# Performance work log

Measured on AMD Instinct MI355X. Metric: run time of the kernel, lower is better.

Reference implementation:

```python
import jax, jax.numpy as jnp
import numpy as np

B, N, M, D, H = 2, 4096, 4096, 512, 8
P = D // H


def setup_inputs() -> dict:
    key = jax.random.key(0)
    ks = jax.random.split(key, 9)
    s = 1.0 / np.sqrt(D)
    return {
        "queries": jax.random.normal(ks[0], (B, N, D), dtype=jnp.float32),
        "keys": jax.random.normal(ks[1], (B, M, D), dtype=jnp.float32),
        "values": jax.random.normal(ks[2], (B, M, D), dtype=jnp.float32),
        "Wq": jax.random.normal(ks[3], (D, D), dtype=jnp.float32) * s,
        "bq": jax.random.normal(ks[4], (D,), dtype=jnp.float32) * s,
        "Wk": jax.random.normal(ks[5], (D, D), dtype=jnp.float32) * s,
        "bk": jax.random.normal(ks[6], (D,), dtype=jnp.float32) * s,
        "Wv": jax.random.normal(ks[7], (D, D), dtype=jnp.float32) * s,
        "bv": jax.random.normal(ks[8], (D,), dtype=jnp.float32) * s,
    }


def reference(queries, keys, values, Wq, bq, Wk, bk, Wv, bv):
    b, n, d = queries.shape
    m = keys.shape[1]
    h, p = H, D // H
    temperature = jnp.asarray(p, queries.dtype) ** 0.5
    # Linear projections (torch Linear: x @ W^T + b; here W stored as [in, out])
    q = (queries @ Wq + bq).reshape(b, n, h, p)
    k = (keys @ Wk + bk).reshape(b, m, h, p)
    v = (values @ Wv + bv).reshape(b, m, h, p)
    # scaled dot-product attention per head; scores [b, h, n, m]
    scores = jnp.einsum("bnhp,bmhp->bhnm", q, k) / temperature
    attn = jax.nn.softmax(scores, axis=-1)
    out = jnp.einsum("bhnm,bmhp->bnhp", attn, v)
    return out.reshape(b, n, d)
```

## Files before the change

kernel.cpp:

```cpp
#include <hip/hip_runtime.h>
#include <stdint.h>

#define B_ 2
#define N_ 4096
#define M_ 4096
#define D_ 512
#define H_ 8
#define P_ 64

typedef short bf16x8 __attribute__((ext_vector_type(8)));
typedef float f32x4 __attribute__((ext_vector_type(4)));
typedef unsigned short u16;
typedef unsigned int u32;
typedef u32 u32x4 __attribute__((ext_vector_type(4)));

static __device__ __forceinline__ u16 f2bf(float f) {
  u32 u = __builtin_bit_cast(u32, f);
  u32 r = u + 0x7fffu + ((u >> 16) & 1u);
  return (u16)(r >> 16);
}

static __device__ __forceinline__ u32 cvtpk(float lo, float hi_) {
  u32 d;
  asm("v_cvt_pk_bf16_f32 %0, %1, %2" : "=v"(d) : "v"(lo), "v"(hi_));
  return d;
}

static __device__ __forceinline__ float fexp2(float x) {
  float r;
  asm("v_exp_f32 %0, %1" : "=v"(r) : "v"(x));
  return r;
}

static __device__ __forceinline__ u32 permpk(const bf16x8& a0, const bf16x8& a1, int i) {
  u32x4 a0w = __builtin_bit_cast(u32x4, a0);
  u32x4 a1w = __builtin_bit_cast(u32x4, a1);
  int wd = i >> 1;
  u32 sel = (i & 1) ? 0x07060302u : 0x05040100u;
  return __builtin_amdgcn_perm(a1w[wd], a0w[wd], sel);
}

__global__ __launch_bounds__(256) void wt_kernel(const float* __restrict__ Wq,
                                                 const float* __restrict__ Wk,
                                                 const float* __restrict__ Wv,
                                                 u16* __restrict__ Wt) {
  __shared__ float tile[32][33];
  int z = blockIdx.z;
  const float* W = (z == 0) ? Wq : (z == 1) ? Wk : Wv;
  u16* out = Wt + (size_t)z * D_ * D_;
  int o0 = blockIdx.x * 32, d0 = blockIdx.y * 32;
  int tx = threadIdx.x, ty = threadIdx.y;
#pragma unroll
  for (int k = 0; k < 4; k++) tile[ty + k * 8][tx] = W[(size_t)(d0 + ty + k * 8) * D_ + o0 + tx];
  __syncthreads();
#pragma unroll
  for (int k = 0; k < 4; k++) out[(size_t)(o0 + ty + k * 8) * D_ + d0 + tx] = f2bf(tile[tx][ty + k * 8]);
}

__global__ __launch_bounds__(256) void proj_kernel(const float* __restrict__ Xq,
                                                   const float* __restrict__ Xk,
                                                   const float* __restrict__ Xv,
                                                   const u16* __restrict__ Wt,
                                                   const float* __restrict__ bq,
                                                   const float* __restrict__ bk,
                                                   const float* __restrict__ bv,
                                                   u16* __restrict__ QKV) {
  int z = blockIdx.z;
  const float* X = (z == 0) ? Xq : (z == 1) ? Xk : Xv;
  const float* bias = (z == 0) ? bq : (z == 1) ? bk : bv;
  const u16* W = Wt + (size_t)z * D_ * D_;
  u16* Y = QKV + (size_t)z * (B_ * N_ * D_);
  const float scale = (z == 0) ? 0.18033688011112042f : 1.0f;

  __shared__ u16 Alds[128 * 32];
  __shared__ u16 Blds[128 * 32];

  int t = threadIdx.x;
  int lane = t & 63, w = t >> 6;
  int wm = w >> 1, wn = w & 1;
  int l15 = lane & 15, g = lane >> 4;
  int rb = blockIdx.y * 128, ob = blockIdx.x * 128;

  const f32x4 zero4 = {0.f, 0.f, 0.f, 0.f};
  f32x4 acc[4][4];
#pragma unroll
  for (int m = 0; m < 4; m++)
#pragma unroll
    for (int n = 0; n < 4; n++) acc[m][n] = zero4;

  for (int kb = 0; kb < D_; kb += 32) {
    __syncthreads();
#pragma unroll
    for (int i = 0; i < 4; i++) {
      int chunk = t + i * 256;
      int row = chunk >> 3, c4 = chunk & 7;
      const float4 v = *(const float4*)&X[(size_t)(rb + row) * D_ + kb + c4 * 4];
      u32 lo = (u32)f2bf(v.x) | ((u32)f2bf(v.y) << 16);
      u32 hi = (u32)f2bf(v.z) | ((u32)f2bf(v.w) << 16);
      int byte = row * 64 + ((c4 * 8) ^ ((row & 3) << 4));
      uint2 d;
      d.x = lo;
      d.y = hi;
      *(uint2*)((char*)Alds + byte) = d;
    }
#pragma unroll
    for (int i = 0; i < 2; i++) {
      int chunk = t + i * 256;
      int row = chunk >> 2, c = chunk & 3;
      bf16x8 v = *(const bf16x8*)&W[(size_t)(ob + row) * D_ + kb + c * 8];
      int byte = row * 64 + ((c * 16) ^ ((row & 3) << 4));
      *(bf16x8*)((char*)Blds + byte) = v;
    }
    __syncthreads();

    bf16x8 a[4], b[4];
#pragma unroll
    for (int m = 0; m < 4; m++) {
      int row = wm * 64 + m * 16 + l15;
      int byte = row * 64 + ((g * 16) ^ ((row & 3) << 4));
      a[m] = *(const bf16x8*)((char*)Alds + byte);
    }
#pragma unroll
    for (int n = 0; n < 4; n++) {
      int row = wn * 64 + n * 16 + l15;
      int byte = row * 64 + ((g * 16) ^ ((row & 3) << 4));
      b[n] = *(const bf16x8*)((char*)Blds + byte);
    }
#pragma unroll
    for (int m = 0; m < 4; m++)
#pragma unroll
      for (int n = 0; n < 4; n++)
        acc[m][n] = __builtin_amdgcn_mfma_f32_16x16x32_bf16(a[m], b[n], acc[m][n], 0, 0, 0);
  }

#pragma unroll
  for (int n = 0; n < 4; n++) {
    int col = ob + wn * 64 + n * 16 + l15;
    float bv_ = bias[col];
#pragma unroll
    for (int m = 0; m < 4; m++) {
      int row0 = rb + wm * 64 + m * 16 + g * 4;
#pragma unroll
      for (int r = 0; r < 4; r++) {
        float y = (acc[m][n][r] + bv_) * scale;
        Y[(size_t)(row0 + r) * D_ + col] = f2bf(y);
      }
    }
  }
}

__global__ __launch_bounds__(256, 2) void attn_kernel(const u16* __restrict__ QKV,
                                                      float* __restrict__ out) {
  const u16* Q = QKV;
  const u16* K = QKV + (size_t)(B_ * N_ * D_);
  const u16* V = K + (size_t)(B_ * N_ * D_);

  __shared__ u16 Klds[2][64 * 64];
  __shared__ u16 Vlds[2][64 * 64];

  char* KL = (char*)&Klds[0][0];
  char* VL = (char*)&Vlds[0][0];

  int t = threadIdx.x, l = t & 63, w = t >> 6;
  int l15 = l & 15, g = (l >> 4) & 3;
  int swz = (l15 & 7) << 4;

  int bid = blockIdx.x + 32 * (blockIdx.y + 8 * blockIdx.z);
  int sbid = (bid & 7) * 64 + (bid >> 3);
  int qt = sbid & 31, h = (sbid >> 5) & 7, b = sbid >> 8;
  int qwa = qt * 128 + w * 16;
  int qwb = qwa + 64;

  const u16* Kb = K + (size_t)(b * M_) * D_ + h * P_;
  const u16* Vb = V + (size_t)(b * M_) * D_ + h * P_;

  bf16x8 qfa[2], qfb[2];
  const u16* qrow_a = Q + (size_t)(b * N_ + qwa + l15) * D_ + h * P_;
  const u16* qrow_b = Q + (size_t)(b * N_ + qwb + l15) * D_ + h * P_;
#pragma unroll
  for (int step = 0; step < 2; step++) {
    qfa[step] = *(const bf16x8*)(qrow_a + step * 32 + g * 8);
    qfb[step] = *(const bf16x8*)(qrow_b + step * 32 + g * 8);
  }

  int koff0 = l15 * 128 + ((g * 16) ^ swz);
  int koff1 = l15 * 128 + ((64 + g * 16) ^ swz);
  int voff0 = koff0, voff1 = koff1;
  int krow = t >> 3, kc = t & 7;
  int kwoff = krow * 128 + ((kc * 16) ^ ((krow & 7) << 4));
  const u16* kg0 = Kb + (size_t)krow * D_ + kc * 8;
  const u16* kg1 = kg0 + (size_t)32 * D_;
  int kp = t & 31, p0 = (t >> 5) * 8;
  int kv0 = 2 * kp, blk = kv0 >> 5, ww_ = kv0 & 31;
  int slot = blk * 32 + ((ww_ >> 2) & 3) * 8 + ((ww_ >> 4) << 2) + (ww_ & 3);
  int vwB = p0 * 128 + 2 * slot;
  const u16* vg0 = Vb + (size_t)kv0 * D_ + p0;
  const u16* vg1 = vg0 + D_;

  const f32x4 zero4 = {0.f, 0.f, 0.f, 0.f};
  const u32x4 onesw = {0x3F803F80u, 0x3F803F80u, 0x3F803F80u, 0x3F803F80u};
  const bf16x8 ones_f = __builtin_bit_cast(bf16x8, onesw);
  f32x4 oa[4], ob_[4], ol_a = zero4, ol_b = zero4;
#pragma unroll
  for (int i = 0; i < 4; i++) {
    oa[i] = zero4;
    ob_[i] = zero4;
  }

  {
    *(bf16x8*)(KL + kwoff) = *(const bf16x8*)kg0;
    *(bf16x8*)(KL + kwoff + 4096) = *(const bf16x8*)kg1;
    bf16x8 a0 = *(const bf16x8*)vg0;
    bf16x8 a1 = *(const bf16x8*)vg1;
#pragma unroll
    for (int i = 0; i < 8; i++) *(u32*)(VL + ((vwB ^ (i << 4)) + i * 128)) = permpk(a0, a1, i);
  }
  kwoff ^= 0x2000;
  vwB ^= 0x2000;
  const u16* kgp0 = kg0 + (size_t)64 * D_;
  const u16* kgp1 = kg1 + (size_t)64 * D_;
  const u16* vgp0 = vg0 + (size_t)64 * D_;
  const u16* vgp1 = vg1 + (size_t)64 * D_;
  __syncthreads();

  const int NT = M_ / 64;
  for (int kt = 0; kt < NT; kt++) {
    bf16x8 kn0 = {}, kn1 = {}, vn0 = {}, vn1 = {};
    if (kt + 1 < NT) {
      kn0 = *(const bf16x8*)kgp0;
      kn1 = *(const bf16x8*)kgp1;
      vn0 = *(const bf16x8*)vgp0;
      vn1 = *(const bf16x8*)vgp1;
      kgp0 += (size_t)64 * D_;
      kgp1 += (size_t)64 * D_;
      vgp0 += (size_t)64 * D_;
      vgp1 += (size_t)64 * D_;
    }

    f32x4 sa[4], sb[4];
#pragma unroll
    for (int i = 0; i < 4; i++) {
      sa[i] = zero4;
      sb[i] = zero4;
    }
    __builtin_amdgcn_s_setprio(1);
#pragma unroll
    for (int tt = 0; tt < 4; tt++) {
      bf16x8 kf0 = *(const bf16x8*)(KL + koff0 + tt * 2048);
      sa[tt] = __builtin_amdgcn_mfma_f32_16x16x32_bf16(kf0, qfa[0], sa[tt], 0, 0, 0);
      sb[tt] = __builtin_amdgcn_mfma_f32_16x16x32_bf16(kf0, qfb[0], sb[tt], 0, 0, 0);
      bf16x8 kf1 = *(const bf16x8*)(KL + koff1 + tt * 2048);
      sa[tt] = __builtin_amdgcn_mfma_f32_16x16x32_bf16(kf1, qfa[1], sa[tt], 0, 0, 0);
      sb[tt] = __builtin_amdgcn_mfma_f32_16x16x32_bf16(kf1, qfb[1], sb[tt], 0, 0, 0);
    }
    __builtin_amdgcn_s_setprio(0);

#pragma unroll
    for (int tt = 0; tt < 4; tt++)
#pragma unroll
      for (int r = 0; r < 4; r++) {
        sa[tt][r] = fexp2(sa[tt][r]);
        sb[tt][r] = fexp2(sb[tt][r]);
      }

    u32 pwa[2][4], pwb[2][4];
#pragma unroll
    for (int kb2 = 0; kb2 < 2; kb2++)
#pragma unroll
      for (int wd = 0; wd < 4; wd++) {
        const f32x4& sva = sa[2 * kb2 + (wd >> 1)];
        const f32x4& svb = sb[2 * kb2 + (wd >> 1)];
        pwa[kb2][wd] = cvtpk(sva[(wd & 1) * 2], sva[(wd & 1) * 2 + 1]);
        pwb[kb2][wd] = cvtpk(svb[(wd & 1) * 2], svb[(wd & 1) * 2 + 1]);
      }

    __builtin_amdgcn_s_setprio(1);
#pragma unroll
    for (int kb2 = 0; kb2 < 2; kb2++) {
      u32x4 pva = {pwa[kb2][0], pwa[kb2][1], pwa[kb2][2], pwa[kb2][3]};
      u32x4 pvb = {pwb[kb2][0], pwb[kb2][1], pwb[kb2][2], pwb[kb2][3]};
      bf16x8 pfa = __builtin_bit_cast(bf16x8, pva);
      bf16x8 pfb = __builtin_bit_cast(bf16x8, pvb);
      int voff = kb2 ? voff1 : voff0;
#pragma unroll
      for (int tt = 0; tt < 4; tt++) {
        bf16x8 vf = *(const bf16x8*)(VL + voff + tt * 2048);
        oa[tt] = __builtin_amdgcn_mfma_f32_16x16x32_bf16(vf, pfa, oa[tt], 0, 0, 0);
        ob_[tt] = __builtin_amdgcn_mfma_f32_16x16x32_bf16(vf, pfb, ob_[tt], 0, 0, 0);
      }
      ol_a = __builtin_amdgcn_mfma_f32_16x16x32_bf16(ones_f, pfa, ol_a, 0, 0, 0);
      ol_b = __builtin_amdgcn_mfma_f32_16x16x32_bf16(ones_f, pfb, ol_b, 0, 0, 0);
    }
    __builtin_amdgcn_s_setprio(0);

    if (kt + 1 < NT) {
      *(bf16x8*)(KL + kwoff) = kn0;
      *(bf16x8*)(KL + kwoff + 4096) = kn1;
#pragma unroll
      for (int i = 0; i < 8; i++) *(u32*)(VL + ((vwB ^ (i << 4)) + i * 128)) = permpk(vn0, vn1, i);
    }
    koff0 ^= 0x2000;
    koff1 ^= 0x2000;
    voff0 ^= 0x2000;
    voff1 ^= 0x2000;
    kwoff ^= 0x2000;
    vwB ^= 0x2000;
    __syncthreads();
  }

  float rla = 1.0f / ol_a[0], rlb = 1.0f / ol_b[0];
  float* orow_a = out + (size_t)(b * N_ + qwa + l15) * D_ + h * P_;
  float* orow_b = out + (size_t)(b * N_ + qwb + l15) * D_ + h * P_;
#pragma unroll
  for (int tt = 0; tt < 4; tt++) {
    float4 sta = {oa[tt][0] * rla, oa[tt][1] * rla, oa[tt][2] * rla, oa[tt][3] * rla};
    *(float4*)(orow_a + tt * 16 + g * 4) = sta;
    float4 stb = {ob_[tt][0] * rlb, ob_[tt][1] * rlb, ob_[tt][2] * rlb, ob_[tt][3] * rlb};
    *(float4*)(orow_b + tt * 16 + g * 4) = stb;
  }
}

extern "C" void kernel_launch(void* const* d_in, const int* in_sizes, int n_in,
                              void* d_out, int out_size, void* d_ws, size_t ws_size,
                              hipStream_t stream) {
  const float* queries = (const float*)d_in[0];
  const float* keys = (const float*)d_in[1];
  const float* values = (const float*)d_in[2];
  const float* Wq = (const float*)d_in[3];
  const float* bq = (const float*)d_in[4];
  const float* Wk = (const float*)d_in[5];
  const float* bk = (const float*)d_in[6];
  const float* Wv = (const float*)d_in[7];
  const float* bv = (const float*)d_in[8];
  float* out = (float*)d_out;

  u16* QKV = (u16*)d_ws;
  u16* Wt = QKV + (size_t)3 * B_ * N_ * D_;

  wt_kernel<<<dim3(16, 16, 3), dim3(32, 8), 0, stream>>>(Wq, Wk, Wv, Wt);
  proj_kernel<<<dim3(4, 64, 3), 256, 0, stream>>>(queries, keys, values, Wt, bq, bk, bv, QKV);
  attn_kernel<<<dim3(32, 8, 2), 256, 0, stream>>>(QKV, out);
}
```

Measured before the change: 119.1 us.

## Double attention block to 512 threads and split K/V tile loading across halves

The attention kernel now runs 8 waves per block covering 256 query rows, half the previous number of blocks, so each K/V tile staged in LDS serves twice as many queries. The first 256 threads load K and the second 256 load and permute V, which halves the per-thread global loads and LDS stores. The score MFMAs now take the zero accumulator directly instead of zeroing registers first. In exchange the grid shrinks to 256 blocks, which can leave some of the GPU's compute units idle, and the launch bound of 512 threads with 2 blocks per CU constrains registers.

```diff
diff --git a/kernel.cpp b/kernel.cpp
--- a/kernel.cpp
+++ b/kernel.cpp
@@ -149,7 +149,7 @@
   }
 }
 
-__global__ __launch_bounds__(256, 2) void attn_kernel(const u16* __restrict__ QKV,
+__global__ __launch_bounds__(512, 2) void attn_kernel(const u16* __restrict__ QKV,
                                                       float* __restrict__ out) {
   const u16* Q = QKV;
   const u16* K = QKV + (size_t)(B_ * N_ * D_);
@@ -165,11 +165,11 @@
   int l15 = l & 15, g = (l >> 4) & 3;
   int swz = (l15 & 7) << 4;
 
-  int bid = blockIdx.x + 32 * (blockIdx.y + 8 * blockIdx.z);
-  int sbid = (bid & 7) * 64 + (bid >> 3);
-  int qt = sbid & 31, h = (sbid >> 5) & 7, b = sbid >> 8;
-  int qwa = qt * 128 + w * 16;
-  int qwb = qwa + 64;
+  int bid = blockIdx.x + 16 * (blockIdx.y + 8 * blockIdx.z);
+  int sbid = (bid & 7) * 32 + (bid >> 3);
+  int qt = sbid & 15, h = (sbid >> 4) & 7, b = sbid >> 7;
+  int qwa = qt * 256 + w * 16;
+  int qwb = qwa + 128;
 
   const u16* Kb = K + (size_t)(b * M_) * D_ + h * P_;
   const u16* Vb = V + (size_t)(b * M_) * D_ + h * P_;
@@ -186,30 +186,34 @@
   int koff0 = l15 * 128 + ((g * 16) ^ swz);
   int koff1 = l15 * 128 + ((64 + g * 16) ^ swz);
   int voff0 = koff0, voff1 = koff1;
-  int krow = t >> 3, kc = t & 7;
+
+  int th = t & 255;
+  bool isK = (t < 256);
+  int krow = th >> 3, kc = th & 7;
   int kwoff = krow * 128 + ((kc * 16) ^ ((krow & 7) << 4));
   const u16* kg0 = Kb + (size_t)krow * D_ + kc * 8;
   const u16* kg1 = kg0 + (size_t)32 * D_;
-  int kp = t & 31, p0 = (t >> 5) * 8;
+  int kp = th & 31, p0 = (th >> 5) * 8;
   int kv0 = 2 * kp, blk = kv0 >> 5, ww_ = kv0 & 31;
   int slot = blk * 32 + ((ww_ >> 2) & 3) * 8 + ((ww_ >> 4) << 2) + (ww_ & 3);
   int vwB = p0 * 128 + 2 * slot;
   const u16* vg0 = Vb + (size_t)kv0 * D_ + p0;
   const u16* vg1 = vg0 + D_;
 
-  const f32x4 zero4 = {0.f, 0.f, 0.f, 0.f};
+  const f32x4 zc = {0.f, 0.f, 0.f, 0.f};
   const u32x4 onesw = {0x3F803F80u, 0x3F803F80u, 0x3F803F80u, 0x3F803F80u};
   const bf16x8 ones_f = __builtin_bit_cast(bf16x8, onesw);
-  f32x4 oa[4], ob_[4], ol_a = zero4, ol_b = zero4;
+  f32x4 oa[4], ob_[4], ol_a = zc, ol_b = zc;
 #pragma unroll
   for (int i = 0; i < 4; i++) {
-    oa[i] = zero4;
-    ob_[i] = zero4;
-  }
-
-  {
+    oa[i] = zc;
+    ob_[i] = zc;
+  }
+
+  if (isK) {
     *(bf16x8*)(KL + kwoff) = *(const bf16x8*)kg0;
     *(bf16x8*)(KL + kwoff + 4096) = *(const bf16x8*)kg1;
+  } else {
     bf16x8 a0 = *(const bf16x8*)vg0;
     bf16x8 a1 = *(const bf16x8*)vg1;
 #pragma unroll
@@ -225,12 +229,15 @@
 
   const int NT = M_ / 64;
   for (int kt = 0; kt < NT; kt++) {
-    bf16x8 kn0 = {}, kn1 = {}, vn0 = {}, vn1 = {};
+    bf16x8 n0 = {}, n1 = {};
     if (kt + 1 < NT) {
-      kn0 = *(const bf16x8*)kgp0;
-      kn1 = *(const bf16x8*)kgp1;
-      vn0 = *(const bf16x8*)vgp0;
-      vn1 = *(const bf16x8*)vgp1;
+      if (isK) {
+        n0 = *(const bf16x8*)kgp0;
+        n1 = *(const bf16x8*)kgp1;
+      } else {
+        n0 = *(const bf16x8*)vgp0;
+        n1 = *(const bf16x8*)vgp1;
+      }
       kgp0 += (size_t)64 * D_;
       kgp1 += (size_t)64 * D_;
       vgp0 += (size_t)64 * D_;
@@ -238,17 +245,12 @@
     }
 
     f32x4 sa[4], sb[4];
-#pragma unroll
-    for (int i = 0; i < 4; i++) {
-      sa[i] = zero4;
-      sb[i] = zero4;
-    }
     __builtin_amdgcn_s_setprio(1);
 #pragma unroll
     for (int tt = 0; tt < 4; tt++) {
       bf16x8 kf0 = *(const bf16x8*)(KL + koff0 + tt * 2048);
-      sa[tt] = __builtin_amdgcn_mfma_f32_16x16x32_bf16(kf0, qfa[0], sa[tt], 0, 0, 0);
-      sb[tt] = __builtin_amdgcn_mfma_f32_16x16x32_bf16(kf0, qfb[0], sb[tt], 0, 0, 0);
+      sa[tt] = __builtin_amdgcn_mfma_f32_16x16x32_bf16(kf0, qfa[0], zc, 0, 0, 0);
+      sb[tt] = __builtin_amdgcn_mfma_f32_16x16x32_bf16(kf0, qfb[0], zc, 0, 0, 0);
       bf16x8 kf1 = *(const bf16x8*)(KL + koff1 + tt * 2048);
       sa[tt] = __builtin_amdgcn_mfma_f32_16x16x32_bf16(kf1, qfa[1], sa[tt], 0, 0, 0);
       sb[tt] = __builtin_amdgcn_mfma_f32_16x16x32_bf16(kf1, qfb[1], sb[tt], 0, 0, 0);
@@ -294,10 +296,13 @@
     __builtin_amdgcn_s_setprio(0);
 
     if (kt + 1 < NT) {
-      *(bf16x8*)(KL + kwoff) = kn0;
-      *(bf16x8*)(KL + kwoff + 4096) = kn1;
-#pragma unroll
-      for (int i = 0; i < 8; i++) *(u32*)(VL + ((vwB ^ (i << 4)) + i * 128)) = permpk(vn0, vn1, i);
+      if (isK) {
+        *(bf16x8*)(KL + kwoff) = n0;
+        *(bf16x8*)(KL + kwoff + 4096) = n1;
+      } else {
+#pragma unroll
+        for (int i = 0; i < 8; i++) *(u32*)(VL + ((vwB ^ (i << 4)) + i * 128)) = permpk(n0, n1, i);
+      }
     }
     koff0 ^= 0x2000;
     koff1 ^= 0x2000;
@@ -339,5 +344,5 @@
 
   wt_kernel<<<dim3(16, 16, 3), dim3(32, 8), 0, stream>>>(Wq, Wk, Wv, Wt);
   proj_kernel<<<dim3(4, 64, 3), 256, 0, stream>>>(queries, keys, values, Wt, bq, bk, bv, QKV);
-  attn_kernel<<<dim3(32, 8, 2), 256, 0, stream>>>(QKV, out);
-}
+  attn_kernel<<<dim3(16, 8, 2), 512, 0, stream>>>(QKV, out);
+}
```

Result: no change. 117.7 us (-1.1%).
